# Kernel optimization log

Measured on AMD Instinct MI355X. Metric: run time of the kernel, lower is better.

Reference implementation:

```python
import jax, jax.numpy as jnp
import numpy as np
import math

B, DIN, H, W = 8, 192, 32, 32
K, DH = 4096, 32

def setup_inputs() -> dict:
    key = jax.random.key(0)
    ks = jax.random.split(key, 8)
    latent = jax.random.normal(ks[0], (B, DIN, H, W), dtype=jnp.float32)
    # kaiming-uniform-ish codebook
    bound = math.sqrt(6.0 / DH)
    codebook = jax.random.uniform(ks[1], (K, DH), minval=-bound, maxval=bound, dtype=jnp.float32)
    wv_w = jax.random.normal(ks[2], (DH, DIN), dtype=jnp.float32) / math.sqrt(DIN)
    wv_b = jax.random.normal(ks[3], (DH,), dtype=jnp.float32) * 0.01
    wq_w = jax.random.normal(ks[4], (DIN, DH), dtype=jnp.float32) / math.sqrt(DH)
    wq_b = jax.random.normal(ks[5], (DIN,), dtype=jnp.float32) * 0.01
    temp1 = jnp.ones((), dtype=jnp.float32)
    u = jax.random.uniform(ks[6], (B, H, W, K), minval=1e-7, maxval=1.0 - 1e-7, dtype=jnp.float32)
    gumbel = -jnp.log(-jnp.log(u))
    return {"latent": latent, "codebook": codebook, "wv_w": wv_w, "wv_b": wv_b,
            "wq_w": wq_w, "wq_b": wq_b, "temp1": temp1, "gumbel": gumbel,
            "temperature": 1}

def _get_logit(x, c):
    x2 = jnp.sum(x * x, axis=-1, keepdims=True)
    c2 = jnp.sum(c * c, axis=-1)
    inter = jnp.einsum('bhwd,kd->bhwk', x, c)
    return -(x2 + c2 - 2.0 * inter)

def reference(latent, codebook, wv_w, wv_b, wq_w, wq_b, temp1, gumbel, temperature):
    q = jnp.transpose(latent, (0, 2, 3, 1))           # [B,H,W,DIN]
    raw = jnp.einsum('bhwi,oi->bhwo', q, wv_w) + wv_b  # [B,H,W,DH]
    logitRaw = _get_logit(raw, codebook)               # [B,H,W,K]
    t = jnp.float32(temperature)
    logit = logitRaw / (temp1 * t)
    trueCode = jnp.argmax(logit, axis=-1)
    tau = jnp.sqrt(t)
    y_soft = jax.nn.softmax((logit + gumbel) / tau, axis=-1)
    y_hard = jax.nn.one_hot(jnp.argmax(y_soft, axis=-1), logit.shape[-1], dtype=y_soft.dtype)
    sample = y_soft + jax.lax.stop_gradient(y_hard - y_soft)  # straight-through
    code = jnp.argmax(sample, axis=-1)
    quantized = jnp.einsum('bhwk,kd->bhwd', sample, codebook)  # [B,H,W,DH]
    hard = jnp.einsum('bhwd,od->bhwo', quantized, wq_w) + wq_b  # [B,H,W,DIN]
    hard = jnp.transpose(hard, (0, 3, 1, 2))                    # [B,DIN,H,W]
    return hard, code, trueCode, logitRaw, raw, quantized, codebook
```

## Files before the change

kernel.cpp:

```cpp
#include <hip/hip_runtime.h>
#include <math.h>

#define NPIX 8192
#define KCB  4096
#define DH   32
#define DIN  192
#define PB   2
#define EPS  2e-3f

__global__ void k_prep(const float* __restrict__ cb, double* __restrict__ c2d,
                       float* __restrict__ c2f, float4* __restrict__ cbT4) {
  int k = blockIdx.x * 256 + threadIdx.x;
  const float4* rp = (const float4*)(cb + k * DH);
  double s = 0.0;
  #pragma unroll
  for (int j = 0; j < DH / 4; ++j) {
    float4 v = rp[j];
    cbT4[j * KCB + k] = v;
    s = fma((double)v.x, (double)v.x, s);
    s = fma((double)v.y, (double)v.y, s);
    s = fma((double)v.z, (double)v.z, s);
    s = fma((double)v.w, (double)v.w, s);
  }
  c2d[k] = s;
  c2f[k] = (float)s;
}

__global__ void k_copy(const float* __restrict__ src, float* __restrict__ dst) {
  int i = blockIdx.x * 256 + threadIdx.x;
  dst[i] = src[i];
}

__global__ __launch_bounds__(256) void k_raw(const float* __restrict__ latent,
    const float* __restrict__ wv_w, const float* __restrict__ wv_b,
    float* __restrict__ raw_out, float* __restrict__ x2_out) {
  __shared__ float wv[DH * 193];
  for (int idx = threadIdx.x; idx < DH * DIN; idx += 256) {
    int o = idx / DIN, i = idx - o * DIN;
    wv[o * 193 + i] = wv_w[idx];
  }
  __syncthreads();
  const int p = blockIdx.x * 8 + (threadIdx.x >> 5);
  const int o = threadIdx.x & 31;
  const int b = p >> 10, hw = p & 1023;
  const float* lp = latent + b * (DIN * 1024) + hw;
  float acc = wv_b[o];
  #pragma unroll 8
  for (int i = 0; i < DIN; ++i) acc = fmaf(lp[i * 1024], wv[o * 193 + i], acc);
  raw_out[p * DH + o] = acc;
  float s = acc * acc;
  #pragma unroll
  for (int m = 16; m; m >>= 1) s += __shfl_xor(s, m, 64);
  if (o == 0) x2_out[p] = s;
}

__device__ inline unsigned long long packkey(float v, int idx) {
  unsigned int u = __float_as_uint(v);
  u = (u & 0x80000000u) ? ~u : (u | 0x80000000u);
  return ((unsigned long long)u << 32) | (unsigned int)(~idx);
}

__device__ inline float rfl(float x) {
  return __uint_as_float(__builtin_amdgcn_readfirstlane(__float_as_uint(x)));
}

__global__ __launch_bounds__(256) void k_main(
    const float* __restrict__ raw_g, const float* __restrict__ x2_g,
    const float4* __restrict__ cbT4, const float* __restrict__ cb,
    const float* __restrict__ c2f, const float* __restrict__ gumbel,
    const float* __restrict__ temp1p, const int* __restrict__ tempp,
    float* __restrict__ logit_out, float* __restrict__ code_out,
    float* __restrict__ true_out, float* __restrict__ quant_out,
    int* __restrict__ flags) {
  __shared__ unsigned long long redk[2][PB][4];
  __shared__ float              redb[2][2][PB][4];
  __shared__ int code_s[PB];

  const int tid  = threadIdx.x;
  const int pix0 = blockIdx.x * PB;

  float sr[PB][DH];
  #pragma unroll
  for (int p = 0; p < PB; ++p)
    #pragma unroll
    for (int d = 0; d < DH; ++d)
      sr[p][d] = rfl(raw_g[(pix0 + p) * DH + d]);

  const float inv_tt = rfl((float)(1.0 / ((double)(*temp1p) * (double)(*tempp))));
  float x2r[PB];
  int   rb[PB];
  #pragma unroll
  for (int p = 0; p < PB; ++p) {
    x2r[p] = rfl(x2_g[pix0 + p]);
    rb[p]  = (pix0 + p) * KCB;
  }

  float bl[PB], bl2[PB], bg[PB], bg2[PB];
  int   bli[PB], bgi[PB];
  #pragma unroll
  for (int p = 0; p < PB; ++p) {
    bl[p] = -INFINITY; bl2[p] = -INFINITY;
    bg[p] = -INFINITY; bg2[p] = -INFINITY;
    bli[p] = 0; bgi[p] = 0;
  }

  float gfc[PB], gfn[PB];
  float c2c, c2n;
  c2c = c2f[tid];
  #pragma unroll
  for (int p = 0; p < PB; ++p) gfc[p] = gumbel[rb[p] + tid];

  #pragma unroll 1
  for (int c = 0; c < 16; ++c) {
    const int k = c * 256 + tid;

    if (c < 15) {
      c2n = c2f[k + 256];
      #pragma unroll
      for (int p = 0; p < PB; ++p) gfn[p] = gumbel[rb[p] + k + 256];
    }

    float4 cv[8];
    #pragma unroll
    for (int j = 0; j < 8; ++j) cv[j] = cbT4[j * KCB + k];

    float dots[PB];
    #pragma unroll
    for (int p = 0; p < PB; ++p) dots[p] = 0.f;
    #pragma unroll
    for (int j = 0; j < 8; ++j) {
      #pragma unroll
      for (int p = 0; p < PB; ++p) {
        dots[p] = fmaf(cv[j].x, sr[p][4 * j + 0], dots[p]);
        dots[p] = fmaf(cv[j].y, sr[p][4 * j + 1], dots[p]);
        dots[p] = fmaf(cv[j].z, sr[p][4 * j + 2], dots[p]);
        dots[p] = fmaf(cv[j].w, sr[p][4 * j + 3], dots[p]);
      }
    }

    #pragma unroll
    for (int p = 0; p < PB; ++p) {
      float v = fmaf(2.f, dots[p], -(x2r[p] + c2c));
      __builtin_nontemporal_store(v, &logit_out[rb[p] + k]);
      bool bt = v > bl[p];
      bl2[p] = bt ? bl[p] : fmaxf(bl2[p], v);
      bli[p] = bt ? k : bli[p];
      bl[p]  = bt ? v : bl[p];
      float z = fmaf(v, inv_tt, gfc[p]);
      bool gt = z > bg[p];
      bg2[p] = gt ? bg[p] : fmaxf(bg2[p], z);
      bgi[p] = gt ? k : bgi[p];
      bg[p]  = gt ? z : bg[p];
    }

    c2c = c2n;
    #pragma unroll
    for (int p = 0; p < PB; ++p) gfc[p] = gfn[p];
  }

  const int wave = tid >> 6;
  const int lane = tid & 63;
  #pragma unroll
  for (int p = 0; p < PB; ++p) {
    unsigned long long kl = packkey(bl[p], bli[p]);
    unsigned long long kg = packkey(bg[p], bgi[p]);
    float b1l = bl[p], b2l = bl2[p], b1g = bg[p], b2g = bg2[p];
    #pragma unroll
    for (int m = 32; m; m >>= 1) {
      unsigned long long o1 = __shfl_xor(kl, m, 64);
      float ob1 = __shfl_xor(b1l, m, 64), ob2 = __shfl_xor(b2l, m, 64);
      b2l = fmaxf(fmaxf(b2l, ob2), fminf(b1l, ob1));
      b1l = fmaxf(b1l, ob1);
      if (o1 > kl) kl = o1;
      unsigned long long o2 = __shfl_xor(kg, m, 64);
      float og1 = __shfl_xor(b1g, m, 64), og2 = __shfl_xor(b2g, m, 64);
      b2g = fmaxf(fmaxf(b2g, og2), fminf(b1g, og1));
      b1g = fmaxf(b1g, og1);
      if (o2 > kg) kg = o2;
    }
    if (lane == 0) {
      redk[0][p][wave] = kl;  redk[1][p][wave] = kg;
      redb[0][0][p][wave] = b1l; redb[0][1][p][wave] = b2l;
      redb[1][0][p][wave] = b1g; redb[1][1][p][wave] = b2g;
    }
  }
  __syncthreads();
  if (tid < PB) {
    const int p = tid;
    unsigned long long kl = redk[0][p][0], kg = redk[1][p][0];
    float b1l = redb[0][0][p][0], b2l = redb[0][1][p][0];
    float b1g = redb[1][0][p][0], b2g = redb[1][1][p][0];
    #pragma unroll
    for (int w2 = 1; w2 < 4; ++w2) {
      if (redk[0][p][w2] > kl) kl = redk[0][p][w2];
      if (redk[1][p][w2] > kg) kg = redk[1][p][w2];
      b2l = fmaxf(fmaxf(b2l, redb[0][1][p][w2]), fminf(b1l, redb[0][0][p][w2]));
      b1l = fmaxf(b1l, redb[0][0][p][w2]);
      b2g = fmaxf(fmaxf(b2g, redb[1][1][p][w2]), fminf(b1g, redb[1][0][p][w2]));
      b1g = fmaxf(b1g, redb[1][0][p][w2]);
    }
    int ti = (int)(~(unsigned int)kl);
    int ci = (int)(~(unsigned int)kg);
    true_out[pix0 + p] = (float)ti;
    code_out[pix0 + p] = (float)ci;
    code_s[p] = ci;
    flags[pix0 + p] = (b1l - b2l < EPS || b1g - b2g < EPS) ? 1 : 0;
  }
  __syncthreads();
  if (tid < PB * DH)
    quant_out[pix0 * DH + tid] = cb[code_s[tid >> 5] * DH + (tid & 31)];
}

__global__ __launch_bounds__(256) void k_refine(
    const float* __restrict__ latent, const float* __restrict__ wv_w,
    const float* __restrict__ wv_b, const float* __restrict__ cb,
    const double* __restrict__ c2d, const float* __restrict__ gumbel,
    const float* __restrict__ temp1p, const int* __restrict__ tempp,
    float* __restrict__ code_out, float* __restrict__ true_out,
    float* __restrict__ quant_out, const int* __restrict__ flags) {
  const int pix = blockIdx.x;
  if (flags[pix] == 0) return;

  __shared__ double part[DH][8];
  __shared__ double rawd[DH];
  __shared__ double x2sh;
  __shared__ double redv[2][4];
  __shared__ int    redi[2][4];
  __shared__ int    ig_sh;
  const int tid = threadIdx.x;
  const int b = pix >> 10, hw = pix & 1023;

  {
    const int o = tid >> 3, pt = tid & 7;
    const float* lp = latent + b * (DIN * 1024) + hw;
    double acc = 0.0;
    #pragma unroll 4
    for (int i = pt * 24; i < pt * 24 + 24; ++i)
      acc = fma((double)lp[i * 1024], (double)wv_w[o * DIN + i], acc);
    part[o][pt] = acc;
  }
  __syncthreads();
  if (tid < DH) {
    double acc = (double)wv_b[tid];
    #pragma unroll
    for (int j = 0; j < 8; ++j) acc += part[tid][j];
    rawd[tid] = acc;
  }
  __syncthreads();
  if (tid == 0) {
    double s = 0.0;
    #pragma unroll
    for (int d = 0; d < DH; ++d) s = fma(rawd[d], rawd[d], s);
    x2sh = s;
  }
  __syncthreads();

  const double tt  = (double)(*temp1p) * (double)(*tempp);
  const double tau = sqrt((double)(*tempp));
  const double x2  = x2sh;

  double bl = -INFINITY, bg = -INFINITY;
  int il = 0, ig = 0;
  for (int c = 0; c < KCB / 256; ++c) {
    const int k = c * 256 + tid;
    const float4* rp = (const float4*)(cb + k * DH);
    double dot = 0.0;
    #pragma unroll
    for (int j = 0; j < DH / 4; ++j) {
      float4 v = rp[j];
      dot = fma((double)v.x, rawd[4 * j + 0], dot);
      dot = fma((double)v.y, rawd[4 * j + 1], dot);
      dot = fma((double)v.z, rawd[4 * j + 2], dot);
      dot = fma((double)v.w, rawd[4 * j + 3], dot);
    }
    double lraw = -((x2 + c2d[k]) - 2.0 * dot);
    double zt = lraw / tt;
    if (zt > bl) { bl = zt; il = k; }
    double zg = (zt + (double)gumbel[(long long)pix * KCB + k]) / tau;
    if (zg > bg) { bg = zg; ig = k; }
  }

  const int wave = tid >> 6, lane = tid & 63;
  #pragma unroll
  for (int m = 32; m; m >>= 1) {
    double ov = __shfl_xor(bl, m, 64); int oi = __shfl_xor(il, m, 64);
    if (ov > bl || (ov == bl && oi < il)) { bl = ov; il = oi; }
    double og = __shfl_xor(bg, m, 64); int oj = __shfl_xor(ig, m, 64);
    if (og > bg || (og == bg && oj < ig)) { bg = og; ig = oj; }
  }
  if (lane == 0) { redv[0][wave] = bl; redi[0][wave] = il;
                   redv[1][wave] = bg; redi[1][wave] = ig; }
  __syncthreads();
  if (tid == 0) {
    double vl = redv[0][0], vg = redv[1][0];
    int    jl = redi[0][0], jg = redi[1][0];
    for (int w2 = 1; w2 < 4; ++w2) {
      if (redv[0][w2] > vl || (redv[0][w2] == vl && redi[0][w2] < jl)) { vl = redv[0][w2]; jl = redi[0][w2]; }
      if (redv[1][w2] > vg || (redv[1][w2] == vg && redi[1][w2] < jg)) { vg = redv[1][w2]; jg = redi[1][w2]; }
    }
    true_out[pix] = (float)jl;
    code_out[pix] = (float)jg;
    ig_sh = jg;
  }
  __syncthreads();
  if (tid < DH) quant_out[pix * DH + tid] = cb[ig_sh * DH + tid];
}

__global__ __launch_bounds__(256) void k_hard(const float* __restrict__ quant,
    const float* __restrict__ wq_w, const float* __restrict__ wq_b,
    float* __restrict__ hard) {
  __shared__ float wq[DIN * DH];
  __shared__ float qs[32][33];
  const int bh = blockIdx.x;
  const int b = bh >> 5, h = bh & 31;
  for (int idx = threadIdx.x; idx < DIN * DH; idx += 256) wq[idx] = wq_w[idx];
  for (int idx = threadIdx.x; idx < 32 * DH; idx += 256)
    qs[idx >> 5][idx & 31] = quant[bh * (32 * DH) + idx];
  __syncthreads();
  for (int it = 0; it < (DIN * 32) / 256; ++it) {
    const int idx = it * 256 + threadIdx.x;
    const int o = idx >> 5, w = idx & 31;
    float acc = wq_b[o];
    #pragma unroll
    for (int d = 0; d < DH; ++d) acc = fmaf(qs[w][d], wq[o * DH + d], acc);
    hard[((b * DIN + o) * 32 + h) * 32 + w] = acc;
  }
}

extern "C" void kernel_launch(void* const* d_in, const int* in_sizes, int n_in,
                              void* d_out, int out_size, void* d_ws, size_t ws_size,
                              hipStream_t stream) {
  const float* latent      = (const float*)d_in[0];
  const float* cb          = (const float*)d_in[1];
  const float* wv_w        = (const float*)d_in[2];
  const float* wv_b        = (const float*)d_in[3];
  const float* wq_w        = (const float*)d_in[4];
  const float* wq_b        = (const float*)d_in[5];
  const float* temp1       = (const float*)d_in[6];
  const float* gumbel      = (const float*)d_in[7];
  const int*   temperature = (const int*)d_in[8];

  float* out      = (float*)d_out;
  float* hard     = out;
  float* code     = out + 1572864;
  float* true_c   = out + 1581056;
  float* logitRaw = out + 1589248;
  float* raw      = out + 35143680;
  float* quant    = out + 35405824;
  float* cb_out   = out + 35668096;

  char*   ws    = (char*)d_ws;
  double* c2d   = (double*)ws;
  float*  c2f   = (float*)(ws + 32768);
  int*    flags = (int*)(ws + 49152);
  float*  x2f   = (float*)(ws + 81920);
  float4* cbT4  = (float4*)(ws + 131072);

  k_prep<<<KCB / 256, 256, 0, stream>>>(cb, c2d, c2f, cbT4);
  k_copy<<<(KCB * DH) / 256, 256, 0, stream>>>(cb, cb_out);
  k_raw <<<NPIX / 8, 256, 0, stream>>>(latent, wv_w, wv_b, raw, x2f);
  k_main<<<NPIX / PB, 256, 0, stream>>>(raw, x2f, cbT4, cb, c2f, gumbel,
                                        temp1, temperature, logitRaw,
                                        code, true_c, quant, flags);
  k_refine<<<NPIX, 256, 0, stream>>>(latent, wv_w, wv_b, cb, c2d, gumbel,
                                     temp1, temperature, code, true_c, quant, flags);
  k_hard<<<8 * 32, 256, 0, stream>>>(quant, wq_w, wq_b, hard);
}
```

Before: 167.7 us.

## Process four pixels per block, keeping two pixel vectors in VGPRs

Each block now handles four pixels instead of two, so every codebook column loaded from global memory is reused across four dot products. The first two pixels' vectors stay in scalar registers via readfirstlane. The other two are loaded into vector registers, with an asm barrier stopping the compiler from scalarizing them, which avoids exceeding the SGPR budget. This roughly halves codebook traffic and grid size, at the cost of extra VGPR pressure and fewer blocks to spread across the GPU.

Result: faster. 144.6 us, median of 2 (-13.8%).

```diff
diff --git a/kernel.cpp b/kernel.cpp
--- a/kernel.cpp
+++ b/kernel.cpp
@@ -5,7 +5,7 @@
 #define KCB  4096
 #define DH   32
 #define DIN  192
-#define PB   2
+#define PB   4
 #define EPS  2e-3f
 
 __global__ void k_prep(const float* __restrict__ cb, double* __restrict__ c2d,
@@ -79,12 +79,23 @@
   const int tid  = threadIdx.x;
   const int pix0 = blockIdx.x * PB;
 
-  float sr[PB][DH];
-  #pragma unroll
-  for (int p = 0; p < PB; ++p)
+  float sr[2][DH];
+  #pragma unroll
+  for (int p = 0; p < 2; ++p)
     #pragma unroll
     for (int d = 0; d < DH; ++d)
       sr[p][d] = rfl(raw_g[(pix0 + p) * DH + d]);
+
+  float vr[2][DH];
+  #pragma unroll
+  for (int p = 0; p < 2; ++p)
+    #pragma unroll
+    for (int j = 0; j < DH / 4; ++j) {
+      float4 t = *(const float4*)&raw_g[(pix0 + 2 + p) * DH + 4 * j];
+      asm("" : "+v"(t.x), "+v"(t.y), "+v"(t.z), "+v"(t.w));
+      vr[p][4 * j + 0] = t.x; vr[p][4 * j + 1] = t.y;
+      vr[p][4 * j + 2] = t.z; vr[p][4 * j + 3] = t.w;
+    }
 
   const float inv_tt = rfl((float)(1.0 / ((double)(*temp1p) * (double)(*tempp))));
   float x2r[PB];
@@ -129,13 +140,22 @@
     for (int p = 0; p < PB; ++p) dots[p] = 0.f;
     #pragma unroll
     for (int j = 0; j < 8; ++j) {
-      #pragma unroll
-      for (int p = 0; p < PB; ++p) {
-        dots[p] = fmaf(cv[j].x, sr[p][4 * j + 0], dots[p]);
-        dots[p] = fmaf(cv[j].y, sr[p][4 * j + 1], dots[p]);
-        dots[p] = fmaf(cv[j].z, sr[p][4 * j + 2], dots[p]);
-        dots[p] = fmaf(cv[j].w, sr[p][4 * j + 3], dots[p]);
-      }
+      dots[0] = fmaf(cv[j].x, sr[0][4 * j + 0], dots[0]);
+      dots[0] = fmaf(cv[j].y, sr[0][4 * j + 1], dots[0]);
+      dots[0] = fmaf(cv[j].z, sr[0][4 * j + 2], dots[0]);
+      dots[0] = fmaf(cv[j].w, sr[0][4 * j + 3], dots[0]);
+      dots[1] = fmaf(cv[j].x, sr[1][4 * j + 0], dots[1]);
+      dots[1] = fmaf(cv[j].y, sr[1][4 * j + 1], dots[1]);
+      dots[1] = fmaf(cv[j].z, sr[1][4 * j + 2], dots[1]);
+      dots[1] = fmaf(cv[j].w, sr[1][4 * j + 3], dots[1]);
+      dots[2] = fmaf(cv[j].x, vr[0][4 * j + 0], dots[2]);
+      dots[2] = fmaf(cv[j].y, vr[0][4 * j + 1], dots[2]);
+      dots[2] = fmaf(cv[j].z, vr[0][4 * j + 2], dots[2]);
+      dots[2] = fmaf(cv[j].w, vr[0][4 * j + 3], dots[2]);
+      dots[3] = fmaf(cv[j].x, vr[1][4 * j + 0], dots[3]);
+      dots[3] = fmaf(cv[j].y, vr[1][4 * j + 1], dots[3]);
+      dots[3] = fmaf(cv[j].z, vr[1][4 * j + 2], dots[3]);
+      dots[3] = fmaf(cv[j].w, vr[1][4 * j + 3], dots[3]);
     }
 
     #pragma unroll
```
